# Optimization experiments

Hardware: AMD Instinct MI355X
Metric: run time of the kernel (lower is better)

## Reference

```python
import jax, jax.numpy as jnp
import numpy as np

N_NODES = 100000
N_EDGES = 1600000
N_GRAPHS = 256
DIMS = [128, 128, 128, 128]  # gcn_layers_dim -> 3 GCNConv layers


def setup_inputs() -> dict:
    key = jax.random.key(0)
    ks = jax.random.split(key, 12)
    inp = {
        "x": jax.random.normal(ks[0], (N_NODES, DIMS[0]), jnp.float32),
        "edge_index": jax.random.randint(ks[1], (2, N_EDGES), 0, N_NODES),
        "edge_weight": jax.random.uniform(ks[2], (N_EDGES,), jnp.float32),
        "batch": jnp.sort(jax.random.randint(ks[3], (N_NODES,), 0, N_GRAPHS)),
    }
    for i in range(3):
        fan_in = DIMS[i]
        scale = 1.0 / np.sqrt(fan_in)
        inp[f"W{i+1}"] = jax.random.uniform(ks[4 + 2 * i], (DIMS[i], DIMS[i + 1]),
                                             jnp.float32, -scale, scale)
        inp[f"b{i+1}"] = jax.random.uniform(ks[5 + 2 * i], (DIMS[i + 1],),
                                             jnp.float32, -scale, scale)
    return inp


def reference(x, edge_index, edge_weight, batch, W1, b1, W2, b2, W3, b3):
    n = x.shape[0]
    # PyG GCNConv: add self-loops with weight 1, symmetric normalization.
    loop = jnp.arange(n)
    row = jnp.concatenate([edge_index[0], loop])  # source nodes
    col = jnp.concatenate([edge_index[1], loop])  # target nodes (aggregation index)
    w = jnp.concatenate([edge_weight, jnp.ones((n,), x.dtype)])
    deg = jax.ops.segment_sum(w, col, num_segments=n)
    dinv = jnp.where(deg > 0, jax.lax.rsqrt(deg), jnp.zeros_like(deg))
    norm = dinv[row] * w * dinv[col]  # [E+N]

    # global_mean_pool setup
    counts = jax.ops.segment_sum(jnp.ones((n,), x.dtype), batch,
                                 num_segments=N_GRAPHS)
    counts = jnp.maximum(counts, 1.0)[:, None]

    def gcn_conv(h, W, b):
        hl = h @ W                      # linear projection first (PyG order)
        msg = hl[row] * norm[:, None]   # gather + edge scaling
        out = jax.ops.segment_sum(msg, col, num_segments=n)  # scatter-add
        return out + b

    embeddings = []
    h = x
    for W, b in ((W1, b1), (W2, b2), (W3, b3)):
        h = gcn_conv(h, W, b)
        h = jax.nn.relu(h)              # relu_layers_index = [0,1,2]
        emb = jax.ops.segment_sum(h, batch, num_segments=N_GRAPHS) / counts
        embeddings.append(emb)          # gep = global_mean_pool
    return tuple(embeddings)
```

## Files before the change

kernel.cpp:

```cpp
#include <hip/hip_runtime.h>


typedef short short8 __attribute__((ext_vector_type(8)));
typedef float f32x4  __attribute__((ext_vector_type(4)));

__device__ inline unsigned pack_bf16x2(float a, float b) {
    unsigned ua = __float_as_uint(a);
    ua = (ua + 0x7FFFu + ((ua >> 16) & 1u)) >> 16;
    unsigned ub = __float_as_uint(b);
    ub = (ub + 0x7FFFu + ((ub >> 16) & 1u)) >> 16;
    return ua | (ub << 16);
}
__device__ inline ushort bf16_1(float a) {
    unsigned ua = __float_as_uint(a);
    return (ushort)((ua + 0x7FFFu + ((ua >> 16) & 1u)) >> 16);
}
__device__ inline float bf_lo(unsigned u) { return __uint_as_float(u << 16); }
__device__ inline float bf_hi(unsigned u) { return __uint_as_float(u & 0xFFFF0000u); }

__global__ void k_prep(int* __restrict__ cnt, int N,
                       const int* __restrict__ batch, int* __restrict__ gb, int G,
                       const float* __restrict__ W0, const float* __restrict__ W1,
                       const float* __restrict__ W2, ushort* __restrict__ WbT) {
    int id = blockIdx.x * blockDim.x + threadIdx.x;
    if (id < N) cnt[id] = 0;
    if (id <= G) {
        int lo = 0, hi = N;
        while (lo < hi) { int mid = (lo + hi) >> 1; if (batch[mid] < id) lo = mid + 1; else hi = mid; }
        gb[id] = lo;
    }
    if (id < 3 * 16384) {
        int l = id >> 14;
        const float* W = (l == 0) ? W0 : ((l == 1) ? W1 : W2);
        int id2 = id & 16383;
        int n = id2 & 127, k = id2 >> 7;
        WbT[l * 16384 + n * 128 + k] = bf16_1(W[k * 128 + n]);
    }
}

__global__ void k_phase1(const int* __restrict__ ei, int* __restrict__ cnt,
                         int* __restrict__ epos, int E,
                         const float4* __restrict__ x4, uint2* __restrict__ xb2,
                         int nCast) {
    int tid = blockIdx.x * blockDim.x + threadIdx.x;
    if (tid < E) {
        int c = ei[E + tid];
        epos[tid] = atomicAdd(&cnt[c], 1);
    }
    int stride = gridDim.x * blockDim.x;
    for (int i = tid; i < nCast; i += stride) {
        float4 f = x4[i];
        uint2 v;
        v.x = pack_bf16x2(f.x, f.y);
        v.y = pack_bf16x2(f.z, f.w);
        xb2[i] = v;
    }
}

__global__ __launch_bounds__(1024) void k_scan1(const int* __restrict__ cnt,
                                                int* __restrict__ pre,
                                                int* __restrict__ bsum, int n) {
    __shared__ int wsum[16];
    int t = threadIdx.x, lane = t & 63, w = t >> 6;
    int i = blockIdx.x * 1024 + t;
    int v = (i < n) ? cnt[i] : 0;
    int x = v;
#pragma unroll
    for (int off = 1; off < 64; off <<= 1) {
        int y = __shfl_up(x, off, 64);
        if (lane >= off) x += y;
    }
    if (lane == 63) wsum[w] = x;
    __syncthreads();
    int woff = 0, tot = 0;
#pragma unroll
    for (int q = 0; q < 16; q++) { int s = wsum[q]; if (q < w) woff += s; tot += s; }
    if (i < n) pre[i] = woff + x - v;
    if (t == 0) bsum[blockIdx.x] = tot;
}

__global__ __launch_bounds__(128) void k_scan2(int* __restrict__ bsum, int nb,
                                               int* __restrict__ ptrv, int n) {
    __shared__ int ws[2];
    int t = threadIdx.x, lane = t & 63, w = t >> 6;
    int v = (t < nb) ? bsum[t] : 0;
    int x = v;
#pragma unroll
    for (int off = 1; off < 64; off <<= 1) {
        int y = __shfl_up(x, off, 64);
        if (lane >= off) x += y;
    }
    if (lane == 63) ws[w] = x;
    __syncthreads();
    int woff = (w == 1) ? ws[0] : 0;
    int tot = ws[0] + ws[1];
    if (t < nb) bsum[t] = woff + x - v;
    if (t == 0) ptrv[n] = tot;
}

__global__ __launch_bounds__(1024) void k_scan3(const int* __restrict__ pre,
                                                const int* __restrict__ bsum,
                                                int* __restrict__ ptrv, int n) {
    int i = blockIdx.x * 1024 + threadIdx.x;
    if (i >= n) return;
    ptrv[i] = pre[i] + bsum[blockIdx.x];
}

__global__ void k_scatter(const int* __restrict__ ei, const float* __restrict__ ew,
                          const int* __restrict__ ptrv, const int* __restrict__ epos,
                          int2* __restrict__ csr, int E) {
    int e = blockIdx.x * blockDim.x + threadIdx.x;
    if (e >= E) return;
    int r = ei[e];
    int c = ei[E + e];
    int2 v; v.x = r; v.y = __float_as_int(ew[e]);
    csr[ptrv[c] + epos[e]] = v;
}

__global__ __launch_bounds__(256) void k_degdinv(const int2* __restrict__ csr,
                                                 const int* __restrict__ ptrv,
                                                 float* __restrict__ dinv, int N) {
    int node = blockIdx.x * 8 + (threadIdx.x >> 5);
    int j = threadIdx.x & 31;
    if (node >= N) return;
    int e0 = ptrv[node], e1 = ptrv[node + 1];
    float s = (j == 0) ? 1.0f : 0.0f;
    for (int e = e0 + j; e < e1; e += 32) s += __int_as_float(csr[e].y);
#pragma unroll
    for (int off = 1; off < 32; off <<= 1) s += __shfl_xor(s, off, 64);
    if (j == 0) dinv[node] = rsqrtf(s);
}

__global__ __launch_bounds__(256) void k_norm(int2* __restrict__ csr,
                                              const int* __restrict__ ptrv,
                                              const float* __restrict__ dinv, int N) {
    int node = blockIdx.x * 8 + (threadIdx.x >> 5);
    int j = threadIdx.x & 31;
    if (node >= N) return;
    float dc = dinv[node];
    int e0 = ptrv[node], e1 = ptrv[node + 1];
    for (int e = e0 + j; e < e1; e += 32) {
        int2 m = csr[e];
        m.y = __float_as_int(dinv[m.x] * __int_as_float(m.y) * dc);
        csr[e] = m;
    }
}

__global__ __launch_bounds__(256) void k_gemm_mfma(const unsigned* __restrict__ Hb,
                                                   const ushort* __restrict__ WbT,
                                                   unsigned* __restrict__ O, int M) {
    __shared__ unsigned sOut[4 * 32 * 64];
    int lane = threadIdx.x & 63;
    int wv = threadIdx.x >> 6;
    int quad = lane >> 4;
    int mrow = lane & 15;
    int m0 = blockIdx.x * 128 + wv * 32;
    int r0 = m0 + mrow;
    int r1 = r0 + 16;
    int r0c = r0 < M ? r0 : M - 1;
    int r1c = r1 < M ? r1 : M - 1;

    short8 a0[4], a1[4];
#pragma unroll
    for (int s = 0; s < 4; s++) {
        a0[s] = *(const short8*)(Hb + (size_t)r0c * 64 + s * 16 + quad * 4);
        a1[s] = *(const short8*)(Hb + (size_t)r1c * 64 + s * 16 + quad * 4);
    }
    f32x4 acc0[8], acc1[8];
#pragma unroll
    for (int t = 0; t < 8; t++) {
        acc0[t] = (f32x4){0.f, 0.f, 0.f, 0.f};
        acc1[t] = (f32x4){0.f, 0.f, 0.f, 0.f};
    }
#pragma unroll
    for (int s = 0; s < 4; s++) {
#pragma unroll
        for (int t = 0; t < 8; t++) {
            short8 b = *(const short8*)(WbT + (t * 16 + mrow) * 128 + s * 32 + quad * 8);
            acc0[t] = __builtin_amdgcn_mfma_f32_16x16x32_bf16(a0[s], b, acc0[t], 0, 0, 0);
            acc1[t] = __builtin_amdgcn_mfma_f32_16x16x32_bf16(a1[s], b, acc1[t], 0, 0, 0);
        }
    }
    ushort* so = (ushort*)(sOut + wv * 32 * 64);
#pragma unroll
    for (int t = 0; t < 8; t++) {
#pragma unroll
        for (int r = 0; r < 4; r++) {
            int lr = quad * 4 + r;
            int c = t * 16 + mrow;
            so[lr * 128 + c] = bf16_1(acc0[t][r]);
            so[(lr + 16) * 128 + c] = bf16_1(acc1[t][r]);
        }
    }
    __syncthreads();
    const unsigned* si = sOut + wv * 32 * 64;
#pragma unroll 8
    for (int r = 0; r < 32; r++) {
        int row = m0 + r;
        if (row < M) O[(size_t)row * 64 + lane] = si[r * 64 + lane];
    }
}

__global__ __launch_bounds__(256) void k_agg(const unsigned* __restrict__ HL,
                                             const int* __restrict__ ptr,
                                             const int2* __restrict__ csr,
                                             const float* __restrict__ dinv,
                                             const float* __restrict__ bias,
                                             unsigned* __restrict__ Hout, int M) {
    __shared__ int2 sM[4 * 64];
    int node = (int)((blockIdx.x * blockDim.x + threadIdx.x) >> 6);
    if (node >= M) return;
    int lane = threadIdx.x & 63;
    int half = lane >> 5;
    int q = lane & 31;
    int2* mbase = &sM[(threadIdx.x >> 6) * 64];
    int e0 = ptr[node], e1 = ptr[node + 1];
    int deg = e1 - e0;
    int nbv = deg < 64 ? deg : 64;
    if (lane < nbv) mbase[lane] = csr[e0 + lane];
    const uint2* HL2 = (const uint2*)HL;
    float di = dinv[node];
    float sn = (half == 0) ? di * di : 0.f;
    uint2 us = HL2[(size_t)node * 32 + q];
    float a0 = sn * bf_lo(us.x), a1 = sn * bf_hi(us.x);
    float a2 = sn * bf_lo(us.y), a3 = sn * bf_hi(us.y);
    int j = half;
    for (; j + 8 <= nbv; j += 8) {
        int2 m[4]; uint2 u[4];
#pragma unroll
        for (int t = 0; t < 4; t++) m[t] = mbase[j + 2 * t];
#pragma unroll
        for (int t = 0; t < 4; t++) u[t] = HL2[(size_t)m[t].x * 32 + q];
#pragma unroll
        for (int t = 0; t < 4; t++) {
            float nv = __int_as_float(m[t].y);
            a0 += nv * bf_lo(u[t].x); a1 += nv * bf_hi(u[t].x);
            a2 += nv * bf_lo(u[t].y); a3 += nv * bf_hi(u[t].y);
        }
    }
    for (; j < nbv; j += 2) {
        int2 m = mbase[j];
        uint2 u = HL2[(size_t)m.x * 32 + q];
        float nv = __int_as_float(m.y);
        a0 += nv * bf_lo(u.x); a1 += nv * bf_hi(u.x);
        a2 += nv * bf_lo(u.y); a3 += nv * bf_hi(u.y);
    }
    for (int e = e0 + 64 + half; e < e1; e += 2) {
        int2 m = csr[e];
        uint2 u = HL2[(size_t)m.x * 32 + q];
        float nv = __int_as_float(m.y);
        a0 += nv * bf_lo(u.x); a1 += nv * bf_hi(u.x);
        a2 += nv * bf_lo(u.y); a3 += nv * bf_hi(u.y);
    }
    a0 += __shfl_xor(a0, 32, 64);
    a1 += __shfl_xor(a1, 32, 64);
    a2 += __shfl_xor(a2, 32, 64);
    a3 += __shfl_xor(a3, 32, 64);
    float4 bv = ((const float4*)bias)[q];
    float r0 = fmaxf(a0 + bv.x, 0.f);
    float r1 = fmaxf(a1 + bv.y, 0.f);
    float r2 = fmaxf(a2 + bv.z, 0.f);
    float r3 = fmaxf(a3 + bv.w, 0.f);
    if (half == 0) {
        uint2 pv;
        pv.x = pack_bf16x2(r0, r1);
        pv.y = pack_bf16x2(r2, r3);
        ((uint2*)(Hout + (size_t)node * 64))[q] = pv;
    }
}

__global__ __launch_bounds__(256) void k_pool(const unsigned* __restrict__ HB,
                                              const int* __restrict__ gb,
                                              float* __restrict__ outp) {
    __shared__ float part[4][128];
    int g = blockIdx.x;
    int lane = threadIdx.x & 63, w = threadIdx.x >> 6;
    int s = gb[g], e = gb[g + 1];
    float ax = 0.f, ay = 0.f;
    for (int i = s + w; i < e; i += 4) {
        unsigned u = HB[(size_t)i * 64 + lane];
        ax += bf_lo(u); ay += bf_hi(u);
    }
    part[w][lane * 2] = ax;
    part[w][lane * 2 + 1] = ay;
    __syncthreads();
    if (threadIdx.x < 128) {
        float sum = part[0][threadIdx.x] + part[1][threadIdx.x]
                  + part[2][threadIdx.x] + part[3][threadIdx.x];
        float c = (float)(e - s);
        outp[g * 128 + threadIdx.x] = sum / fmaxf(c, 1.0f);
    }
}

extern "C" void kernel_launch(void* const* d_in, const int* in_sizes, int n_in,
                              void* d_out, int out_size, void* d_ws, size_t ws_size,
                              hipStream_t stream) {
    const float* x     = (const float*)d_in[0];
    const int*   ei    = (const int*)d_in[1];
    const float* ew    = (const float*)d_in[2];
    const int*   batch = (const int*)d_in[3];
    const float* Wt[3] = {(const float*)d_in[4], (const float*)d_in[6], (const float*)d_in[8]};
    const float* bt[3] = {(const float*)d_in[5], (const float*)d_in[7], (const float*)d_in[9]};
    float* out = (float*)d_out;

    const int D = 128;
    const int N = in_sizes[0] / D;
    const int E = in_sizes[2];
    const int G = out_size / (3 * D);

    char* p = (char*)d_ws;
    auto alloc = [&](size_t bytes) {
        void* r = (void*)p;
        p += (bytes + 255) & ~(size_t)255;
        return r;
    };
    int*      cnt    = (int*)alloc((size_t)N * 4);
    int*      ptr    = (int*)alloc((size_t)(N + 1) * 4);
    int*      pre    = (int*)alloc((size_t)N * 4);
    int*      bsum   = (int*)alloc((size_t)128 * 4);
    int*      gb     = (int*)alloc((size_t)(G + 1) * 4);
    float*    dinv   = (float*)alloc((size_t)N * 4);
    ushort*   WbT    = (ushort*)alloc((size_t)3 * 16384 * 2);
    int2*     csr    = (int2*)alloc((size_t)E * 8);
    unsigned* xb     = (unsigned*)alloc((size_t)N * 64 * 4);
    unsigned* bufHL  = (unsigned*)alloc((size_t)N * 64 * 4);
    unsigned* bufH   = (unsigned*)alloc((size_t)N * 64 * 4);
    int*      epos   = (int*)bufH;

    int nb = (N + 1023) / 1024;
    int prepWork = N > 3 * 16384 ? N : 3 * 16384;

    k_prep<<<(prepWork + 255) / 256, 256, 0, stream>>>(cnt, N, batch, gb, G,
                                                       Wt[0], Wt[1], Wt[2], WbT);
    k_phase1<<<(E + 255) / 256, 256, 0, stream>>>(ei, cnt, epos, E,
                                                  (const float4*)x, (uint2*)xb, N * 32);
    k_scan1<<<nb, 1024, 0, stream>>>(cnt, pre, bsum, N);
    k_scan2<<<1, 128, 0, stream>>>(bsum, nb, ptr, N);
    k_scan3<<<nb, 1024, 0, stream>>>(pre, bsum, ptr, N);
    k_scatter<<<(E + 255) / 256, 256, 0, stream>>>(ei, ew, ptr, epos, csr, E);
    k_degdinv<<<(N + 7) / 8, 256, 0, stream>>>(csr, ptr, dinv, N);
    k_norm<<<(N + 7) / 8, 256, 0, stream>>>(csr, ptr, dinv, N);

    for (int l = 0; l < 3; l++) {
        const unsigned* hin = (l == 0) ? xb : bufH;
        k_gemm_mfma<<<(N + 127) / 128, 256, 0, stream>>>(hin, WbT + (size_t)l * 16384,
                                                         bufHL, N);
        k_agg<<<(N + 3) / 4, 256, 0, stream>>>(bufHL, ptr, csr, dinv, bt[l], bufH, N);
        k_pool<<<G, 256, 0, stream>>>(bufH, gb, out + (size_t)l * G * D);
    }
}
```

Baseline: 597.0 us.

## Fuse graph-setup kernels into one cooperative persistent kernel with grid syncs

Replaces the eight setup launches (prep, count, three-pass scan, scatter, degree, norm) with a single cooperative kernel of 1024 blocks that uses grid-wide syncs between phases. The scan now uses a 256-thread block partition with a single-block second pass over 1024 block sums. The aim is to remove kernel launch overhead and inter-kernel gaps. The cost is grid-sync latency and a fixed grid size that may under-occupy some phases, and the kernel requires all 1024 blocks to be co-resident.

```diff
diff --git a/kernel.cpp b/kernel.cpp
--- a/kernel.cpp
+++ b/kernel.cpp
@@ -1,8 +1,13 @@
 #include <hip/hip_runtime.h>
+#include <hip/hip_cooperative_groups.h>
+
+namespace cg = cooperative_groups;
 
 
 typedef short short8 __attribute__((ext_vector_type(8)));
 typedef float f32x4  __attribute__((ext_vector_type(4)));
+
+#define SETUP_BLOCKS 1024
 
 __device__ inline unsigned pack_bf16x2(float a, float b) {
     unsigned ua = __float_as_uint(a);
@@ -18,52 +23,50 @@
 __device__ inline float bf_lo(unsigned u) { return __uint_as_float(u << 16); }
 __device__ inline float bf_hi(unsigned u) { return __uint_as_float(u & 0xFFFF0000u); }
 
-__global__ void k_prep(int* __restrict__ cnt, int N,
-                       const int* __restrict__ batch, int* __restrict__ gb, int G,
-                       const float* __restrict__ W0, const float* __restrict__ W1,
-                       const float* __restrict__ W2, ushort* __restrict__ WbT) {
-    int id = blockIdx.x * blockDim.x + threadIdx.x;
-    if (id < N) cnt[id] = 0;
-    if (id <= G) {
+__global__ __launch_bounds__(256) void k_setup(
+        const int* __restrict__ ei, const float* __restrict__ ew,
+        const int* __restrict__ batch,
+        const float* __restrict__ W0, const float* __restrict__ W1,
+        const float* __restrict__ W2, const float4* __restrict__ x4,
+        int* __restrict__ cnt, int* __restrict__ ptrv, int* __restrict__ bsum,
+        int* __restrict__ gb, float* __restrict__ dinv,
+        ushort* __restrict__ WbT, uint2* __restrict__ xb2,
+        int* __restrict__ epos, int2* __restrict__ csr,
+        int N, int E, int G) {
+    cg::grid_group grid = cg::this_grid();
+    const int tid = blockIdx.x * 256 + threadIdx.x;
+    const int nthr = SETUP_BLOCKS * 256;
+
+    for (int i = tid; i < N; i += nthr) cnt[i] = 0;
+    if (tid <= G) {
         int lo = 0, hi = N;
-        while (lo < hi) { int mid = (lo + hi) >> 1; if (batch[mid] < id) lo = mid + 1; else hi = mid; }
-        gb[id] = lo;
-    }
-    if (id < 3 * 16384) {
-        int l = id >> 14;
+        while (lo < hi) { int mid = (lo + hi) >> 1; if (batch[mid] < tid) lo = mid + 1; else hi = mid; }
+        gb[tid] = lo;
+    }
+    for (int i = tid; i < 3 * 16384; i += nthr) {
+        int l = i >> 14;
         const float* W = (l == 0) ? W0 : ((l == 1) ? W1 : W2);
-        int id2 = id & 16383;
+        int id2 = i & 16383;
         int n = id2 & 127, k = id2 >> 7;
         WbT[l * 16384 + n * 128 + k] = bf16_1(W[k * 128 + n]);
     }
-}
-
-__global__ void k_phase1(const int* __restrict__ ei, int* __restrict__ cnt,
-                         int* __restrict__ epos, int E,
-                         const float4* __restrict__ x4, uint2* __restrict__ xb2,
-                         int nCast) {
-    int tid = blockIdx.x * blockDim.x + threadIdx.x;
-    if (tid < E) {
-        int c = ei[E + tid];
-        epos[tid] = atomicAdd(&cnt[c], 1);
-    }
-    int stride = gridDim.x * blockDim.x;
-    for (int i = tid; i < nCast; i += stride) {
+    grid.sync();
+
+    for (int e = tid; e < E; e += nthr)
+        epos[e] = atomicAdd(&cnt[ei[E + e]], 1);
+    for (int i = tid; i < N * 32; i += nthr) {
         float4 f = x4[i];
         uint2 v;
         v.x = pack_bf16x2(f.x, f.y);
         v.y = pack_bf16x2(f.z, f.w);
         xb2[i] = v;
     }
-}
-
-__global__ __launch_bounds__(1024) void k_scan1(const int* __restrict__ cnt,
-                                                int* __restrict__ pre,
-                                                int* __restrict__ bsum, int n) {
-    __shared__ int wsum[16];
-    int t = threadIdx.x, lane = t & 63, w = t >> 6;
-    int i = blockIdx.x * 1024 + t;
-    int v = (i < n) ? cnt[i] : 0;
+    grid.sync();
+
+    __shared__ int wsum[4];
+    __shared__ int btot[256];
+    int lane = threadIdx.x & 63, w = threadIdx.x >> 6;
+    int v = (tid < N) ? cnt[tid] : 0;
     int x = v;
 #pragma unroll
     for (int off = 1; off < 64; off <<= 1) {
@@ -74,75 +77,67 @@
     __syncthreads();
     int woff = 0, tot = 0;
 #pragma unroll
-    for (int q = 0; q < 16; q++) { int s = wsum[q]; if (q < w) woff += s; tot += s; }
-    if (i < n) pre[i] = woff + x - v;
-    if (t == 0) bsum[blockIdx.x] = tot;
-}
-
-__global__ __launch_bounds__(128) void k_scan2(int* __restrict__ bsum, int nb,
-                                               int* __restrict__ ptrv, int n) {
-    __shared__ int ws[2];
-    int t = threadIdx.x, lane = t & 63, w = t >> 6;
-    int v = (t < nb) ? bsum[t] : 0;
-    int x = v;
-#pragma unroll
-    for (int off = 1; off < 64; off <<= 1) {
-        int y = __shfl_up(x, off, 64);
-        if (lane >= off) x += y;
-    }
-    if (lane == 63) ws[w] = x;
-    __syncthreads();
-    int woff = (w == 1) ? ws[0] : 0;
-    int tot = ws[0] + ws[1];
-    if (t < nb) bsum[t] = woff + x - v;
-    if (t == 0) ptrv[n] = tot;
-}
-
-__global__ __launch_bounds__(1024) void k_scan3(const int* __restrict__ pre,
-                                                const int* __restrict__ bsum,
-                                                int* __restrict__ ptrv, int n) {
-    int i = blockIdx.x * 1024 + threadIdx.x;
-    if (i >= n) return;
-    ptrv[i] = pre[i] + bsum[blockIdx.x];
-}
-
-__global__ void k_scatter(const int* __restrict__ ei, const float* __restrict__ ew,
-                          const int* __restrict__ ptrv, const int* __restrict__ epos,
-                          int2* __restrict__ csr, int E) {
-    int e = blockIdx.x * blockDim.x + threadIdx.x;
-    if (e >= E) return;
-    int r = ei[e];
-    int c = ei[E + e];
-    int2 v; v.x = r; v.y = __float_as_int(ew[e]);
-    csr[ptrv[c] + epos[e]] = v;
-}
-
-__global__ __launch_bounds__(256) void k_degdinv(const int2* __restrict__ csr,
-                                                 const int* __restrict__ ptrv,
-                                                 float* __restrict__ dinv, int N) {
-    int node = blockIdx.x * 8 + (threadIdx.x >> 5);
+    for (int q = 0; q < 4; q++) { int s = wsum[q]; if (q < w) woff += s; tot += s; }
+    int myPre = woff + x - v;
+    if (threadIdx.x == 0) bsum[blockIdx.x] = tot;
+    grid.sync();
+
+    if (blockIdx.x == 0) {
+        int t = threadIdx.x;
+        int b4[4];
+#pragma unroll
+        for (int q = 0; q < 4; q++) b4[q] = bsum[t * 4 + q];
+        int s4 = b4[0] + b4[1] + b4[2] + b4[3];
+        int xx = s4;
+#pragma unroll
+        for (int off = 1; off < 64; off <<= 1) {
+            int y = __shfl_up(xx, off, 64);
+            if (lane >= off) xx += y;
+        }
+        if (lane == 63) btot[w] = xx;
+        __syncthreads();
+        int woff2 = 0;
+#pragma unroll
+        for (int q = 0; q < 4; q++) { if (q < w) woff2 += btot[q]; }
+        int off0 = woff2 + xx - s4;
+        int run = off0;
+#pragma unroll
+        for (int q = 0; q < 4; q++) { int bv = b4[q]; bsum[t * 4 + q] = run; run += bv; }
+        if (t == 255) ptrv[N] = run;
+    }
+    grid.sync();
+    if (tid < N) ptrv[tid] = myPre + bsum[blockIdx.x];
+    grid.sync();
+
+    for (int e = tid; e < E; e += nthr) {
+        int r = ei[e];
+        int c = ei[E + e];
+        int2 m; m.x = r; m.y = __float_as_int(ew[e]);
+        csr[ptrv[c] + epos[e]] = m;
+    }
+    grid.sync();
+
+    int hw = tid >> 5;
     int j = threadIdx.x & 31;
-    if (node >= N) return;
-    int e0 = ptrv[node], e1 = ptrv[node + 1];
-    float s = (j == 0) ? 1.0f : 0.0f;
-    for (int e = e0 + j; e < e1; e += 32) s += __int_as_float(csr[e].y);
-#pragma unroll
-    for (int off = 1; off < 32; off <<= 1) s += __shfl_xor(s, off, 64);
-    if (j == 0) dinv[node] = rsqrtf(s);
-}
-
-__global__ __launch_bounds__(256) void k_norm(int2* __restrict__ csr,
-                                              const int* __restrict__ ptrv,
-                                              const float* __restrict__ dinv, int N) {
-    int node = blockIdx.x * 8 + (threadIdx.x >> 5);
-    int j = threadIdx.x & 31;
-    if (node >= N) return;
-    float dc = dinv[node];
-    int e0 = ptrv[node], e1 = ptrv[node + 1];
-    for (int e = e0 + j; e < e1; e += 32) {
-        int2 m = csr[e];
-        m.y = __float_as_int(dinv[m.x] * __int_as_float(m.y) * dc);
-        csr[e] = m;
+    int nhw = nthr >> 5;
+    for (int node = hw; node < N; node += nhw) {
+        int e0 = ptrv[node], e1 = ptrv[node + 1];
+        float s = (j == 0) ? 1.0f : 0.0f;
+        for (int e = e0 + j; e < e1; e += 32) s += __int_as_float(csr[e].y);
+#pragma unroll
+        for (int off = 1; off < 32; off <<= 1) s += __shfl_xor(s, off, 64);
+        if (j == 0) dinv[node] = rsqrtf(s);
+    }
+    grid.sync();
+
+    for (int node = hw; node < N; node += nhw) {
+        float dc = dinv[node];
+        int e0 = ptrv[node], e1 = ptrv[node + 1];
+        for (int e = e0 + j; e < e1; e += 32) {
+            int2 m = csr[e];
+            m.y = __float_as_int(dinv[m.x] * __int_as_float(m.y) * dc);
+            csr[e] = m;
+        }
     }
 }
 
@@ -299,14 +294,16 @@
     const int*   ei    = (const int*)d_in[1];
     const float* ew    = (const float*)d_in[2];
     const int*   batch = (const int*)d_in[3];
-    const float* Wt[3] = {(const float*)d_in[4], (const float*)d_in[6], (const float*)d_in[8]};
+    const float* W0 = (const float*)d_in[4];
+    const float* W1 = (const float*)d_in[6];
+    const float* W2 = (const float*)d_in[8];
     const float* bt[3] = {(const float*)d_in[5], (const float*)d_in[7], (const float*)d_in[9]};
     float* out = (float*)d_out;
 
     const int D = 128;
-    const int N = in_sizes[0] / D;
-    const int E = in_sizes[2];
-    const int G = out_size / (3 * D);
+    int N = in_sizes[0] / D;
+    int E = in_sizes[2];
+    int G = out_size / (3 * D);
 
     char* p = (char*)d_ws;
     auto alloc = [&](size_t bytes) {
@@ -316,8 +313,7 @@
     };
     int*      cnt    = (int*)alloc((size_t)N * 4);
     int*      ptr    = (int*)alloc((size_t)(N + 1) * 4);
-    int*      pre    = (int*)alloc((size_t)N * 4);
-    int*      bsum   = (int*)alloc((size_t)128 * 4);
+    int*      bsum   = (int*)alloc((size_t)SETUP_BLOCKS * 4);
     int*      gb     = (int*)alloc((size_t)(G + 1) * 4);
     float*    dinv   = (float*)alloc((size_t)N * 4);
     ushort*   WbT    = (ushort*)alloc((size_t)3 * 16384 * 2);
@@ -327,19 +323,17 @@
     unsigned* bufH   = (unsigned*)alloc((size_t)N * 64 * 4);
     int*      epos   = (int*)bufH;
 
-    int nb = (N + 1023) / 1024;
-    int prepWork = N > 3 * 16384 ? N : 3 * 16384;
-
-    k_prep<<<(prepWork + 255) / 256, 256, 0, stream>>>(cnt, N, batch, gb, G,
-                                                       Wt[0], Wt[1], Wt[2], WbT);
-    k_phase1<<<(E + 255) / 256, 256, 0, stream>>>(ei, cnt, epos, E,
-                                                  (const float4*)x, (uint2*)xb, N * 32);
-    k_scan1<<<nb, 1024, 0, stream>>>(cnt, pre, bsum, N);
-    k_scan2<<<1, 128, 0, stream>>>(bsum, nb, ptr, N);
-    k_scan3<<<nb, 1024, 0, stream>>>(pre, bsum, ptr, N);
-    k_scatter<<<(E + 255) / 256, 256, 0, stream>>>(ei, ew, ptr, epos, csr, E);
-    k_degdinv<<<(N + 7) / 8, 256, 0, stream>>>(csr, ptr, dinv, N);
-    k_norm<<<(N + 7) / 8, 256, 0, stream>>>(csr, ptr, dinv, N);
+    const float4* x4 = (const float4*)x;
+    uint2* xb2 = (uint2*)xb;
+    void* args[] = {
+        (void*)&ei, (void*)&ew, (void*)&batch,
+        (void*)&W0, (void*)&W1, (void*)&W2, (void*)&x4,
+        (void*)&cnt, (void*)&ptr, (void*)&bsum, (void*)&gb, (void*)&dinv,
+        (void*)&WbT, (void*)&xb2, (void*)&epos, (void*)&csr,
+        (void*)&N, (void*)&E, (void*)&G
+    };
+    hipLaunchCooperativeKernel((const void*)k_setup, dim3(SETUP_BLOCKS), dim3(256),
+                               args, 0, stream);
 
     for (int l = 0; l < 3; l++) {
         const unsigned* hin = (l == 0) ? xb : bufH;
```

After: 1.366 ms. 129% more time.
